# Optimization experiments

Hardware: AMD Instinct MI355X
Metric: run time of the kernel (lower is better)

## Reference

```python
import jax, jax.numpy as jnp
import numpy as np

N = 50000   # nodes
E = 800000  # edges
D = 128     # feature / hidden dim
G = 64      # graphs in batch
L = 3       # GCN layers
EPS = 1e-5  # LayerNorm eps (torch default)


def setup_inputs() -> dict:
    key = jax.random.key(0)
    ks = jax.random.split(key, 6)
    x = jax.random.normal(ks[0], (N, D), dtype=jnp.float32)
    edge_index = jax.random.randint(ks[1], (2, E), 0, N)
    batch = jnp.sort(jax.random.randint(ks[2], (N,), 0, G))
    Ws = jax.random.normal(ks[3], (L, D, D), dtype=jnp.float32) / np.sqrt(D).astype(np.float32)
    bs = jnp.zeros((L, D), dtype=jnp.float32)
    gammas = jnp.ones((L, D), dtype=jnp.float32)
    betas = jnp.zeros((L, D), dtype=jnp.float32)
    return {"x": x, "edge_index": edge_index, "batch": batch,
            "Ws": Ws, "bs": bs, "gammas": gammas, "betas": betas,
            "num_graphs": G}


def _layernorm(h, g, b):
    mu = jnp.mean(h, axis=-1, keepdims=True)
    var = jnp.mean((h - mu) ** 2, axis=-1, keepdims=True)
    return g * (h - mu) * jax.lax.rsqrt(var + EPS) + b


def reference(x, edge_index, batch, Ws, bs, gammas, betas, num_graphs):
    n = x.shape[0]
    loop = jnp.arange(n)
    # GCNConv adds self-loops; symmetric normalization on augmented graph
    src = jnp.concatenate([edge_index[0], loop])
    dst = jnp.concatenate([edge_index[1], loop])
    deg = jax.ops.segment_sum(jnp.ones_like(dst, dtype=x.dtype), dst, num_segments=n)
    dinv = jax.lax.rsqrt(jnp.maximum(deg, 1.0))  # deg >= 1 via self-loops
    norm_e = dinv[src] * dinv[dst]               # [E+N]

    h = x
    for i in range(Ws.shape[0]):
        hw = h @ Ws[i]                           # [N, D] dense GEMM
        msg = hw[src] * norm_e[:, None]          # gather + edge scale
        h = jax.ops.segment_sum(msg, dst, num_segments=n) + bs[i]  # scatter-add
        h = jax.nn.relu(_layernorm(h, gammas[i], betas[i]))
        # dropout is identity in eval mode

    # global mean pool over graph ids
    s = jax.ops.segment_sum(h, batch, num_segments=num_graphs)
    cnt = jax.ops.segment_sum(jnp.ones((n,), x.dtype), batch, num_segments=num_graphs)
    return s / jnp.maximum(cnt, 1.0)[:, None]
```

## Files before the change

### kernel.cpp

```cpp
#include <hip/hip_runtime.h>
#include <math.h>


#define NDIM 128
#define LN_EPS 1e-5f
#define NGRAPH 64
#define EPB 2048

typedef __attribute__((ext_vector_type(8))) short short8;
typedef __attribute__((ext_vector_type(4))) float f32x4;

__device__ __forceinline__ ushort f2bf(float f) {
    unsigned u = __float_as_uint(f);
    return (ushort)((u + 0x7FFF + ((u >> 16) & 1)) >> 16);
}
__device__ __forceinline__ float bf2f(ushort b) {
    return __uint_as_float(((unsigned)b) << 16);
}

__device__ __forceinline__ uint block_excl_scan(uint v, uint* s) {
    int t = threadIdx.x;
    s[t] = v; __syncthreads();
    #pragma unroll
    for (int off = 1; off < 256; off <<= 1) {
        uint x = (t >= off) ? s[t - off] : 0u;
        __syncthreads();
        s[t] += x;
        __syncthreads();
    }
    uint incl = s[t];
    __syncthreads();
    return incl - v;
}


__global__ __launch_bounds__(256) void k_h1(const int* __restrict__ dst, uint* __restrict__ hist, int E) {
    __shared__ uint h[256];
    int t = threadIdx.x, b = blockIdx.x;
    h[t] = 0; __syncthreads();
    int e0 = b * EPB;
    #pragma unroll
    for (int i = 0; i < 8; i++) {
        int e = e0 + i * 256 + t;
        if (e < E) atomicAdd(&h[((uint)dst[e]) >> 8], 1u);
    }
    __syncthreads();
    hist[(size_t)b * 256 + t] = h[t];
}

__global__ __launch_bounds__(256) void k_colscan(uint* __restrict__ hist, uint* __restrict__ colsum, int EB) {
    __shared__ uint s[256];
    int t = threadIdx.x, j = blockIdx.x;
    uint v0 = (2 * t     < EB) ? hist[(size_t)(2 * t) * 256 + j] : 0u;
    uint v1 = (2 * t + 1 < EB) ? hist[(size_t)(2 * t + 1) * 256 + j] : 0u;
    uint pair = v0 + v1;
    uint excl = block_excl_scan(pair, s);
    if (2 * t < EB)     hist[(size_t)(2 * t) * 256 + j] = excl;
    if (2 * t + 1 < EB) hist[(size_t)(2 * t + 1) * 256 + j] = excl + v0;
    if (t == 255) colsum[j] = excl + pair;
}

__global__ __launch_bounds__(256) void k_binscan(const uint* __restrict__ colsum, uint* __restrict__ eoff,
                                                 uint* __restrict__ cbase) {
    __shared__ uint s[256];
    int t = threadIdx.x;
    uint total = colsum[t];
    uint er = block_excl_scan(total, s);
    eoff[t] = er;
    if (t == 255) eoff[256] = er + total;
    uint ep = block_excl_scan((total + 3u) & ~3u, s);
    cbase[t] = ep + 768u * (uint)t;
}

__global__ __launch_bounds__(256) void k_scatter1(const int* __restrict__ src, const int* __restrict__ dst,
                                                  const uint* __restrict__ hist, const uint* __restrict__ eoff,
                                                  uint* __restrict__ ebuf, int E) {
    __shared__ uint off[256];
    __shared__ uint cur[256];
    int t = threadIdx.x, b = blockIdx.x;
    off[t] = eoff[t] + hist[(size_t)b * 256 + t];
    cur[t] = 0;
    __syncthreads();
    int e0 = b * EPB;
    #pragma unroll
    for (int i = 0; i < 8; i++) {
        int e = e0 + i * 256 + t;
        if (e < E) {
            uint d = (uint)dst[e], sv = (uint)src[e];
            uint bin = d >> 8;
            uint r = atomicAdd(&cur[bin], 1u);
            ebuf[off[bin] + r] = (d << 16) | sv;
        }
    }
}

__global__ __launch_bounds__(256) void k_sort2(const uint* __restrict__ ebuf, const uint* __restrict__ eoff,
                                               const uint* __restrict__ cbase, const int* __restrict__ batch,
                                               ushort* __restrict__ csr, int* __restrict__ base,
                                               int* __restrict__ deg, float* __restrict__ dinv,
                                               int* __restrict__ gstart, int* __restrict__ gend, int N) {
    __shared__ uint h[256], nbase[256], s[256];
    int t = threadIdx.x, b = blockIdx.x;
    uint lo = eoff[b];
    int cnt = (int)(eoff[b + 1] - lo);
    h[t] = 0; __syncthreads();
    for (int i = t; i < cnt; i += 256)
        atomicAdd(&h[(ebuf[lo + i] >> 16) & 255u], 1u);
    __syncthreads();
    uint dg = h[t];
    uint excl = block_excl_scan((dg + 3u) & ~3u, s);
    uint myb = cbase[b] + excl;
    nbase[t] = myb;
    int n = b * 256 + t;
    if (n < N) {
        base[n] = (int)myb;
        deg[n] = (int)dg;
        dinv[n] = rsqrtf((float)(dg + 1u));
        int g = batch[n];
        if (n == 0 || batch[n - 1] != g) gstart[g] = n;
        if (n == N - 1 || batch[n + 1] != g) gend[g] = n + 1;
    }
    h[t] = 0;
    __syncthreads();
    for (int i = t; i < cnt; i += 256) {
        uint e = ebuf[lo + i];
        uint bin = (e >> 16) & 255u;
        uint r = atomicAdd(&h[bin], 1u);
        csr[nbase[bin] + r] = (ushort)(e & 0xFFFFu);
    }
}


__global__ __launch_bounds__(256) void k_wt(const float* __restrict__ W, ushort* __restrict__ Wt) {
    int l = blockIdx.x;
    const float* w = W + (size_t)l * NDIM * NDIM;
    char* o = (char*)(Wt + (size_t)l * NDIM * NDIM);
    for (int idx = threadIdx.x; idx < NDIM * NDIM; idx += 256) {
        int k = idx >> 7, n = idx & 127;
        int byte = ((n * NDIM + k) * 2) ^ ((n & 7) << 4);
        *(ushort*)(o + byte) = f2bf(w[idx]);
    }
}


template <bool AF32>
__global__ __launch_bounds__(256) void k_gemm(const void* __restrict__ Ap, const ushort* __restrict__ Wt,
                                              ushort* __restrict__ C, const float* __restrict__ dinv, int N) {
    __shared__ char sW[32768];
    int tid = threadIdx.x;
    {
        const float4* g = (const float4*)Wt;
        float4* s = (float4*)sW;
        #pragma unroll
        for (int i = 0; i < 8; i++) s[tid + 256 * i] = g[tid + 256 * i];
    }
    __syncthreads();

    int wave = tid >> 6, lane = tid & 63;
    int l15 = lane & 15, lhi = lane >> 4;
    int row0 = blockIdx.x * 128 + wave * 32;

    f32x4 acc[2][8];
    #pragma unroll
    for (int m = 0; m < 2; m++)
        #pragma unroll
        for (int n = 0; n < 8; n++) acc[m][n] = f32x4{0.f, 0.f, 0.f, 0.f};

    const float*  Af = (const float*)Ap;
    const ushort* Ab = (const ushort*)Ap;

    #pragma unroll
    for (int ks = 0; ks < 4; ks++) {
        int k = ks * 32 + lhi * 8;
        short8 a[2];
        #pragma unroll
        for (int m = 0; m < 2; m++) {
            int r = row0 + m * 16 + l15;
            if (r < N) {
                if (AF32) {
                    float4 v0 = *(const float4*)&Af[(size_t)r * NDIM + k];
                    float4 v1 = *(const float4*)&Af[(size_t)r * NDIM + k + 4];
                    short8 t;
                    t[0] = (short)f2bf(v0.x); t[1] = (short)f2bf(v0.y);
                    t[2] = (short)f2bf(v0.z); t[3] = (short)f2bf(v0.w);
                    t[4] = (short)f2bf(v1.x); t[5] = (short)f2bf(v1.y);
                    t[6] = (short)f2bf(v1.z); t[7] = (short)f2bf(v1.w);
                    a[m] = t;
                } else {
                    a[m] = *(const short8*)&Ab[(size_t)r * NDIM + k];
                }
            } else {
                a[m] = short8{};
            }
        }
        #pragma unroll
        for (int n = 0; n < 8; n++) {
            int nn = n * 16 + l15;
            int byte = (nn * 256 + k * 2) ^ ((nn & 7) << 4);
            short8 b = *(const short8*)(sW + byte);
            acc[0][n] = __builtin_amdgcn_mfma_f32_16x16x32_bf16(a[0], b, acc[0][n], 0, 0, 0);
            acc[1][n] = __builtin_amdgcn_mfma_f32_16x16x32_bf16(a[1], b, acc[1][n], 0, 0, 0);
        }
    }

    #pragma unroll
    for (int m = 0; m < 2; m++) {
        int rbase = row0 + m * 16 + lhi * 4;
        #pragma unroll
        for (int r = 0; r < 4; r++) {
            int row = rbase + r;
            if (row < N) {
                float dn = dinv[row];
                #pragma unroll
                for (int n = 0; n < 8; n++)
                    C[(size_t)row * NDIM + n * 16 + l15] = f2bf(acc[m][n][r] * dn);
            }
        }
    }
}


__global__ __launch_bounds__(256) void k_agg(const ushort* __restrict__ hw, ushort* __restrict__ out,
                                             const float* __restrict__ dinv, const int* __restrict__ base,
                                             const int* __restrict__ deg, const ushort* __restrict__ csr,
                                             const float* __restrict__ bias, const float* __restrict__ gamma,
                                             const float* __restrict__ beta, int N) {
    int gtid = blockIdx.x * 256 + threadIdx.x;
    int n = gtid >> 5;
    int l4 = threadIdx.x & 31;
    if (n >= N) return;

    const ushort4* hv = (const ushort4*)hw;
    ushort4 sv = hv[(size_t)n * 32 + l4];
    float a0 = bf2f(sv.x), a1 = bf2f(sv.y), a2 = bf2f(sv.z), a3 = bf2f(sv.w);

    int b0 = base[n], dg = deg[n];
    int nfull = dg & ~3;
    ushort4 s4;
    if (nfull > 0) s4 = *(const ushort4*)&csr[b0];
    for (int i = 0; i < nfull; i += 4) {
        ushort4 cur = s4;
        if (i + 4 < nfull) s4 = *(const ushort4*)&csr[b0 + i + 4];
        ushort4 t0 = hv[(size_t)cur.x * 32 + l4];
        ushort4 t1 = hv[(size_t)cur.y * 32 + l4];
        ushort4 t2 = hv[(size_t)cur.z * 32 + l4];
        ushort4 t3 = hv[(size_t)cur.w * 32 + l4];
        a0 += bf2f(t0.x) + bf2f(t1.x) + bf2f(t2.x) + bf2f(t3.x);
        a1 += bf2f(t0.y) + bf2f(t1.y) + bf2f(t2.y) + bf2f(t3.y);
        a2 += bf2f(t0.z) + bf2f(t1.z) + bf2f(t2.z) + bf2f(t3.z);
        a3 += bf2f(t0.w) + bf2f(t1.w) + bf2f(t2.w) + bf2f(t3.w);
    }
    for (int i = nfull; i < dg; i++) {
        int s = csr[b0 + i];
        ushort4 t = hv[(size_t)s * 32 + l4];
        a0 += bf2f(t.x); a1 += bf2f(t.y); a2 += bf2f(t.z); a3 += bf2f(t.w);
    }

    float dn = dinv[n];
    a0 *= dn; a1 *= dn; a2 *= dn; a3 *= dn;

    float4 bv = ((const float4*)bias)[l4];
    a0 += bv.x; a1 += bv.y; a2 += bv.z; a3 += bv.w;

    float s1 = a0 + a1 + a2 + a3;
    float s2 = a0 * a0 + a1 * a1 + a2 * a2 + a3 * a3;
    #pragma unroll
    for (int o = 1; o < 32; o <<= 1) {
        s1 += __shfl_xor(s1, o);
        s2 += __shfl_xor(s2, o);
    }
    float mu = s1 * (1.f / NDIM);
    float var = s2 * (1.f / NDIM) - mu * mu;
    float rs = rsqrtf(var + LN_EPS);

    float4 gv = ((const float4*)gamma)[l4];
    float4 be = ((const float4*)beta)[l4];
    ushort4 y;
    y.x = f2bf(fmaxf(gv.x * (a0 - mu) * rs + be.x, 0.f));
    y.y = f2bf(fmaxf(gv.y * (a1 - mu) * rs + be.y, 0.f));
    y.z = f2bf(fmaxf(gv.z * (a2 - mu) * rs + be.z, 0.f));
    y.w = f2bf(fmaxf(gv.w * (a3 - mu) * rs + be.w, 0.f));
    ((ushort4*)out)[(size_t)n * 32 + l4] = y;
}


__global__ __launch_bounds__(128) void k_pool(const ushort* __restrict__ h, const int* __restrict__ batch,
                                              float* __restrict__ out, int N) {
    int d = threadIdx.x;
    int start = blockIdx.x * 64;
    if (start >= N) return;
    int end = min(start + 64, N);
    int cur = batch[start];
    float sum = 0.f;
    for (int n = start; n < end; n++) {
        int g = batch[n];
        if (g != cur) {
            atomicAdd(&out[cur * NDIM + d], sum);
            sum = 0.f;
            cur = g;
        }
        sum += bf2f(h[(size_t)n * NDIM + d]);
    }
    atomicAdd(&out[cur * NDIM + d], sum);
}

__global__ __launch_bounds__(256) void k_div(float* __restrict__ out, const int* __restrict__ gstart,
                                             const int* __restrict__ gend) {
    int i = blockIdx.x * 256 + threadIdx.x;
    if (i < NGRAPH * NDIM) {
        int g = i >> 7;
        float c = (float)(gend[g] - gstart[g]);
        out[i] /= fmaxf(c, 1.f);
    }
}


extern "C" void kernel_launch(void* const* d_in, const int* in_sizes, int n_in,
                              void* d_out, int out_size, void* d_ws, size_t ws_size,
                              hipStream_t stream) {
    const float* x      = (const float*)d_in[0];
    const int*   ei     = (const int*)d_in[1];
    const int*   batch  = (const int*)d_in[2];
    const float* Ws     = (const float*)d_in[3];
    const float* bs     = (const float*)d_in[4];
    const float* gammas = (const float*)d_in[5];
    const float* betas  = (const float*)d_in[6];
    float* out = (float*)d_out;

    int N = in_sizes[0] / NDIM;
    int E = in_sizes[1] / 2;
    const int* src = ei;
    const int* dst = ei + E;
    int EB = (E + EPB - 1) / EPB;
    int NB = (N + 255) / 256;

    char* w = (char*)d_ws;
    auto alloc = [&](size_t bytes) { char* p = w; w += (bytes + 255) & ~(size_t)255; return p; };
    int*    deg    = (int*)alloc((size_t)N * 4);
    int*    base   = (int*)alloc((size_t)N * 4);
    float*  dinv   = (float*)alloc((size_t)N * 4);
    uint*   hist   = (uint*)alloc((size_t)EB * 256 * 4);
    uint*   colsum = (uint*)alloc(256 * 4);
    uint*   eoff   = (uint*)alloc(257 * 4);
    uint*   cbase  = (uint*)alloc(256 * 4);
    uint*   ebuf   = (uint*)alloc((size_t)E * 4);
    ushort* csr    = (ushort*)alloc(((size_t)E + 256u * 772u) * 2);
    int*    gse    = (int*)alloc(2 * NGRAPH * 4);
    int*    gstart = gse;
    int*    gend   = gse + NGRAPH;
    ushort* Wt     = (ushort*)alloc((size_t)3 * NDIM * NDIM * 2);
    ushort* bufA   = (ushort*)alloc((size_t)N * NDIM * 2);
    ushort* bufB   = (ushort*)alloc((size_t)N * NDIM * 2);

    hipMemsetAsync(out, 0, (size_t)NGRAPH * NDIM * 4, stream);

    k_h1<<<EB, 256, 0, stream>>>(dst, hist, E);
    k_colscan<<<256, 256, 0, stream>>>(hist, colsum, EB);
    k_binscan<<<1, 256, 0, stream>>>(colsum, eoff, cbase);
    k_scatter1<<<EB, 256, 0, stream>>>(src, dst, hist, eoff, ebuf, E);
    k_sort2<<<NB, 256, 0, stream>>>(ebuf, eoff, cbase, batch, csr, base, deg, dinv, gstart, gend, N);
    k_wt<<<3, 256, 0, stream>>>(Ws, Wt);

    int gGemm = (N + 127) / 128;
    int gAgg  = (N * 32 + 255) / 256;
    for (int l = 0; l < 3; l++) {
        const ushort* wl = Wt + (size_t)l * NDIM * NDIM;
        if (l == 0)
            k_gemm<true><<<gGemm, 256, 0, stream>>>((const void*)x, wl, bufB, dinv, N);
        else
            k_gemm<false><<<gGemm, 256, 0, stream>>>((const void*)bufA, wl, bufB, dinv, N);
        k_agg<<<gAgg, 256, 0, stream>>>(bufB, bufA, dinv, base, deg, csr,
                                        bs + l * NDIM, gammas + l * NDIM, betas + l * NDIM, N);
    }

    k_pool<<<(N + 63) / 64, 128, 0, stream>>>(bufA, batch, out, N);
    k_div<<<(NGRAPH * NDIM + 255) / 256, 256, 0, stream>>>(out, gstart, gend);
}
```

Before: 283.2 us.

## Halve GEMM row tile, stage output in LDS, unroll aggregation gather by 8

The GEMM tile drops from 128 to 64 rows per block, giving each wave one 16-row MFMA slab and twice as many blocks. The output is staged through shared memory so global stores become coalesced 16-byte writes instead of scattered 2-byte stores. Separately, the aggregation loop now issues 8 neighbor gathers per iteration instead of 4, to keep more loads in flight. The costs are more shared memory per block, an extra barrier, and a second full load of W into LDS for every additional block, plus more registers in the aggregation kernel.

Result: slower. 290.2 us (+2.5%).

```diff
diff --git a/kernel.cpp b/kernel.cpp
--- a/kernel.cpp
+++ b/kernel.cpp
@@ -147,6 +147,7 @@
 __global__ __launch_bounds__(256) void k_gemm(const void* __restrict__ Ap, const ushort* __restrict__ Wt,
                                               ushort* __restrict__ C, const float* __restrict__ dinv, int N) {
     __shared__ char sW[32768];
+    __shared__ ushort sC[64 * NDIM];
     int tid = threadIdx.x;
     {
         const float4* g = (const float4*)Wt;
@@ -158,13 +159,11 @@
 
     int wave = tid >> 6, lane = tid & 63;
     int l15 = lane & 15, lhi = lane >> 4;
-    int row0 = blockIdx.x * 128 + wave * 32;
-
-    f32x4 acc[2][8];
-    #pragma unroll
-    for (int m = 0; m < 2; m++)
-        #pragma unroll
-        for (int n = 0; n < 8; n++) acc[m][n] = f32x4{0.f, 0.f, 0.f, 0.f};
+    int rw = blockIdx.x * 64 + wave * 16;
+
+    f32x4 acc[8];
+    #pragma unroll
+    for (int n = 0; n < 8; n++) acc[n] = f32x4{0.f, 0.f, 0.f, 0.f};
 
     const float*  Af = (const float*)Ap;
     const ushort* Ab = (const ushort*)Ap;
@@ -172,25 +171,20 @@
     #pragma unroll
     for (int ks = 0; ks < 4; ks++) {
         int k = ks * 32 + lhi * 8;
-        short8 a[2];
-        #pragma unroll
-        for (int m = 0; m < 2; m++) {
-            int r = row0 + m * 16 + l15;
-            if (r < N) {
-                if (AF32) {
-                    float4 v0 = *(const float4*)&Af[(size_t)r * NDIM + k];
-                    float4 v1 = *(const float4*)&Af[(size_t)r * NDIM + k + 4];
-                    short8 t;
-                    t[0] = (short)f2bf(v0.x); t[1] = (short)f2bf(v0.y);
-                    t[2] = (short)f2bf(v0.z); t[3] = (short)f2bf(v0.w);
-                    t[4] = (short)f2bf(v1.x); t[5] = (short)f2bf(v1.y);
-                    t[6] = (short)f2bf(v1.z); t[7] = (short)f2bf(v1.w);
-                    a[m] = t;
-                } else {
-                    a[m] = *(const short8*)&Ab[(size_t)r * NDIM + k];
-                }
+        short8 a = short8{};
+        int r = rw + l15;
+        if (r < N) {
+            if (AF32) {
+                float4 v0 = *(const float4*)&Af[(size_t)r * NDIM + k];
+                float4 v1 = *(const float4*)&Af[(size_t)r * NDIM + k + 4];
+                short8 t;
+                t[0] = (short)f2bf(v0.x); t[1] = (short)f2bf(v0.y);
+                t[2] = (short)f2bf(v0.z); t[3] = (short)f2bf(v0.w);
+                t[4] = (short)f2bf(v1.x); t[5] = (short)f2bf(v1.y);
+                t[6] = (short)f2bf(v1.z); t[7] = (short)f2bf(v1.w);
+                a = t;
             } else {
-                a[m] = short8{};
+                a = *(const short8*)&Ab[(size_t)r * NDIM + k];
             }
         }
         #pragma unroll
@@ -198,24 +192,27 @@
             int nn = n * 16 + l15;
             int byte = (nn * 256 + k * 2) ^ ((nn & 7) << 4);
             short8 b = *(const short8*)(sW + byte);
-            acc[0][n] = __builtin_amdgcn_mfma_f32_16x16x32_bf16(a[0], b, acc[0][n], 0, 0, 0);
-            acc[1][n] = __builtin_amdgcn_mfma_f32_16x16x32_bf16(a[1], b, acc[1][n], 0, 0, 0);
-        }
-    }
-
-    #pragma unroll
-    for (int m = 0; m < 2; m++) {
-        int rbase = row0 + m * 16 + lhi * 4;
+            acc[n] = __builtin_amdgcn_mfma_f32_16x16x32_bf16(a, b, acc[n], 0, 0, 0);
+        }
+    }
+
+    #pragma unroll
+    for (int r = 0; r < 4; r++) {
+        int row = rw + lhi * 4 + r;
+        float dn = (row < N) ? dinv[row] : 0.f;
         #pragma unroll
-        for (int r = 0; r < 4; r++) {
-            int row = rbase + r;
-            if (row < N) {
-                float dn = dinv[row];
-                #pragma unroll
-                for (int n = 0; n < 8; n++)
-                    C[(size_t)row * NDIM + n * 16 + l15] = f2bf(acc[m][n][r] * dn);
-            }
-        }
+        for (int n = 0; n < 8; n++)
+            sC[(wave * 16 + lhi * 4 + r) * NDIM + n * 16 + l15] = f2bf(acc[n][r] * dn);
+    }
+    __syncthreads();
+    int row0 = blockIdx.x * 64;
+    #pragma unroll
+    for (int i = 0; i < 4; i++) {
+        int flat = tid + i * 256;
+        int row = flat >> 4, c8 = (flat & 15) * 8;
+        int gr = row0 + row;
+        if (gr < N)
+            *(short8*)&C[(size_t)gr * NDIM + c8] = *(const short8*)&sC[row * NDIM + c8];
     }
 }
 
@@ -235,20 +232,34 @@
     float a0 = bf2f(sv.x), a1 = bf2f(sv.y), a2 = bf2f(sv.z), a3 = bf2f(sv.w);
 
     int b0 = base[n], dg = deg[n];
-    int nfull = dg & ~3;
-    ushort4 s4;
-    if (nfull > 0) s4 = *(const ushort4*)&csr[b0];
-    for (int i = 0; i < nfull; i += 4) {
-        ushort4 cur = s4;
-        if (i + 4 < nfull) s4 = *(const ushort4*)&csr[b0 + i + 4];
-        ushort4 t0 = hv[(size_t)cur.x * 32 + l4];
-        ushort4 t1 = hv[(size_t)cur.y * 32 + l4];
-        ushort4 t2 = hv[(size_t)cur.z * 32 + l4];
-        ushort4 t3 = hv[(size_t)cur.w * 32 + l4];
-        a0 += bf2f(t0.x) + bf2f(t1.x) + bf2f(t2.x) + bf2f(t3.x);
-        a1 += bf2f(t0.y) + bf2f(t1.y) + bf2f(t2.y) + bf2f(t3.y);
-        a2 += bf2f(t0.z) + bf2f(t1.z) + bf2f(t2.z) + bf2f(t3.z);
-        a3 += bf2f(t0.w) + bf2f(t1.w) + bf2f(t2.w) + bf2f(t3.w);
+    int nfull = dg & ~7;
+    ushort4 sa, sb;
+    if (nfull > 0) {
+        sa = *(const ushort4*)&csr[b0];
+        sb = *(const ushort4*)&csr[b0 + 4];
+    }
+    for (int i = 0; i < nfull; i += 8) {
+        ushort4 ca = sa, cb = sb;
+        if (i + 8 < nfull) {
+            sa = *(const ushort4*)&csr[b0 + i + 8];
+            sb = *(const ushort4*)&csr[b0 + i + 12];
+        }
+        ushort4 t0 = hv[(size_t)ca.x * 32 + l4];
+        ushort4 t1 = hv[(size_t)ca.y * 32 + l4];
+        ushort4 t2 = hv[(size_t)ca.z * 32 + l4];
+        ushort4 t3 = hv[(size_t)ca.w * 32 + l4];
+        ushort4 t4 = hv[(size_t)cb.x * 32 + l4];
+        ushort4 t5 = hv[(size_t)cb.y * 32 + l4];
+        ushort4 t6 = hv[(size_t)cb.z * 32 + l4];
+        ushort4 t7 = hv[(size_t)cb.w * 32 + l4];
+        a0 += bf2f(t0.x) + bf2f(t1.x) + bf2f(t2.x) + bf2f(t3.x)
+            + bf2f(t4.x) + bf2f(t5.x) + bf2f(t6.x) + bf2f(t7.x);
+        a1 += bf2f(t0.y) + bf2f(t1.y) + bf2f(t2.y) + bf2f(t3.y)
+            + bf2f(t4.y) + bf2f(t5.y) + bf2f(t6.y) + bf2f(t7.y);
+        a2 += bf2f(t0.z) + bf2f(t1.z) + bf2f(t2.z) + bf2f(t3.z)
+            + bf2f(t4.z) + bf2f(t5.z) + bf2f(t6.z) + bf2f(t7.z);
+        a3 += bf2f(t0.w) + bf2f(t1.w) + bf2f(t2.w) + bf2f(t3.w)
+            + bf2f(t4.w) + bf2f(t5.w) + bf2f(t6.w) + bf2f(t7.w);
     }
     for (int i = nfull; i < dg; i++) {
         int s = csr[b0 + i];
@@ -361,7 +372,7 @@
     k_sort2<<<NB, 256, 0, stream>>>(ebuf, eoff, cbase, batch, csr, base, deg, dinv, gstart, gend, N);
     k_wt<<<3, 256, 0, stream>>>(Ws, Wt);
 
-    int gGemm = (N + 127) / 128;
+    int gGemm = (N + 63) / 64;
     int gAgg  = (N * 32 + 255) / 256;
     for (int l = 0; l < 3; l++) {
         const ushort* wl = Wt + (size_t)l * NDIM * NDIM;
```
